# Optimization experiments

Measured on AMD Instinct MI355X. Metric: run time of the kernel, lower is better.

The kernel has to match this reference:

```python
import jax, jax.numpy as jnp
import numpy as np

B, T, D = 4, 1024, 256
H, DK, C = 8, 32, 16  # n_heads, d_key, pos-encoder hidden units
DV = D // H
NEG = -1e15
EPS_SM = 1e-5
EPS_LN = 1e-5
SLOPE = 0.01  # LeakyReLU default


def setup_inputs() -> dict:
    key = jax.random.key(0)
    ks = jax.random.split(key, 16)
    s = 0.05
    x = jax.random.normal(ks[0], (B, T, D), jnp.float32)
    src_mask = jax.random.randint(ks[1], (B, T, T), 0, 2).astype(bool)
    rel_dists = jax.random.uniform(ks[2], (B, 1, T, T), jnp.float32)
    Wq = jax.random.normal(ks[3], (H, DK, D), jnp.float32) * s
    Wk = jax.random.normal(ks[4], (H, DK, D), jnp.float32) * s
    Wv = jax.random.normal(ks[5], (H, DV, D), jnp.float32) * s
    pw1 = jax.random.normal(ks[6], (H, C), jnp.float32) * s
    pb1 = jax.random.normal(ks[7], (H, C), jnp.float32) * s
    pw2 = jax.random.normal(ks[8], (H, C), jnp.float32) * s
    pb2 = jax.random.normal(ks[9], (H,), jnp.float32) * s
    Wo = jax.random.normal(ks[10], (D, D), jnp.float32) * s
    bo = jax.random.normal(ks[11], (D,), jnp.float32) * s
    Wf = jax.random.normal(ks[12], (D, D), jnp.float32) * s
    bf = jax.random.normal(ks[13], (D,), jnp.float32) * s
    g1 = jnp.ones((D,), jnp.float32)
    beta1 = jnp.zeros((D,), jnp.float32)
    g2 = jnp.ones((D,), jnp.float32)
    beta2 = jnp.zeros((D,), jnp.float32)
    return dict(x=x, src_mask=src_mask, rel_dists=rel_dists, Wq=Wq, Wk=Wk, Wv=Wv,
                pw1=pw1, pb1=pb1, pw2=pw2, pb2=pb2, Wo=Wo, bo=bo, Wf=Wf, bf=bf,
                g1=g1, beta1=beta1, g2=g2, beta2=beta2)


def _l2norm(v):
    # F.normalize(p=2, dim=-1): v / max(||v||, 1e-12)
    n = jnp.sqrt(jnp.sum(v * v, axis=-1, keepdims=True))
    return v / jnp.maximum(n, 1e-12)


def _lrelu(h):
    return jnp.where(h >= 0, h, SLOPE * h)


def _pos_bias(d, pw1, pb1, pw2, pb2):
    # d: [B,T,T]; per-head 1x1-conv MLP applied elementwise.
    # Loop over the tiny channel dim (16) to avoid a [B,H,T,T,C] intermediate.
    bias = jnp.broadcast_to(pb2[None, :, None, None], (d.shape[0], pw1.shape[0], d.shape[1], d.shape[2]))
    for c in range(pw1.shape[1]):
        h = d[:, None] * pw1[None, :, c, None, None] + pb1[None, :, c, None, None]
        bias = bias + pw2[None, :, c, None, None] * _lrelu(h)
    return bias  # [B,H,T,T]


def _layer_norm(v, g, b):
    mu = jnp.mean(v, axis=-1, keepdims=True)
    var = jnp.mean((v - mu) ** 2, axis=-1, keepdims=True)
    return (v - mu) * jax.lax.rsqrt(var + EPS_LN) * g + b


def reference(x, src_mask, rel_dists, Wq, Wk, Wv, pw1, pb1, pw2, pb2,
              Wo, bo, Wf, bf, g1, beta1, g2, beta2):
    # cosine-normalized multi-head attention (all heads batched)
    q = _l2norm(jnp.einsum('btd,hkd->bhtk', x, Wq))
    k = _l2norm(jnp.einsum('bsd,hkd->bhsk', x, Wk))
    v = jnp.einsum('bsd,hvd->bhsv', x, Wv)
    logits = jnp.einsum('bhtk,bhsk->bhts', q, k)
    logits = logits - _pos_bias(rel_dists[:, 0], pw1, pb1, pw2, pb2)
    logits = jnp.where(src_mask[:, None], NEG, logits)
    # custom softmax: exp / (sum + 1e-5) (handles all-padded rows)
    z = jnp.exp(logits)
    attn = z / (jnp.sum(z, axis=-1, keepdims=True) + EPS_SM)
    heads = jnp.einsum('bhts,bhsv->bhtv', attn, v)
    y = heads.transpose(0, 2, 1, 3).reshape(x.shape[0], x.shape[1], -1)  # concat heads
    y = y @ Wo.T + bo
    # residual + LN + FFN (dropout is identity in eval mode)
    zz = _layer_norm(x + y, g1, beta1)
    z_ff = _lrelu(zz @ Wf.T + bf)
    return _layer_norm(zz + z_ff, g2, beta2)
```

## Files before the change

### kernel.cpp

```cpp
#include <hip/hip_runtime.h>
#include <math.h>

#define Tc 1024
#define Dc 256
#define Hc 8
#define Cc 16
#define LUTN 256

typedef __attribute__((ext_vector_type(8))) short short8;
typedef __attribute__((ext_vector_type(4))) float f32x4;

__device__ __forceinline__ unsigned bf16u(float x) {
    unsigned u = __float_as_uint(x);
    return (u + 0x7FFFu + ((u >> 16) & 1u)) >> 16;
}
__device__ __forceinline__ unsigned pk2(float lo, float hi) {
    return bf16u(lo) | (bf16u(hi) << 16);
}
__device__ __forceinline__ unsigned pk2t(float lo, float hi) {
    return __builtin_amdgcn_perm(__float_as_uint(hi), __float_as_uint(lo), 0x07060302u);
}
__device__ __forceinline__ float upk(unsigned v) { return __uint_as_float(v << 16); }
__device__ __forceinline__ float upkh(unsigned v) { return __uint_as_float(v & 0xffff0000u); }

__global__ __launch_bounds__(256) void cast_all(
    const float* __restrict__ rel, const int* __restrict__ msk,
    const float* __restrict__ Wq, const float* __restrict__ Wk,
    const float* __restrict__ Wv, const float* __restrict__ Wo,
    const float* __restrict__ Wf,
    const float* __restrict__ pw1, const float* __restrict__ pb1,
    const float* __restrict__ pw2, const float* __restrict__ pb2,
    ushort* __restrict__ Wqkvc, ushort* __restrict__ Woc,
    ushort* __restrict__ Wfc, ushort* __restrict__ LUTb,
    ushort* __restrict__ Dm)
{
    const int bid = blockIdx.x;
    const int tid = threadIdx.x;
    if (bid == 320) {
        const int bin = tid;
        const float d0 = bin * (1.f / LUTN), d1 = (bin + 1) * (1.f / LUTN);
        for (int h = 0; h < Hc; ++h) {
            float y0 = pb2[h], y1 = pb2[h];
#pragma unroll
            for (int c = 0; c < Cc; ++c) {
                float w1 = pw1[h * Cc + c], b1 = pb1[h * Cc + c], w2 = pw2[h * Cc + c];
                float h0 = fmaf(w1, d0, b1), h1 = fmaf(w1, d1, b1);
                y0 = fmaf(w2, h0 >= 0.f ? h0 : 0.01f * h0, y0);
                y1 = fmaf(w2, h1 >= 0.f ? h1 : 0.01f * h1, y1);
            }
            float a = (y1 - y0) * (float)LUTN;
            float b = y0 - a * d0;
            LUTb[(h >> 1) * 1024 + bin * 4 + (h & 1) * 2]     = (ushort)bf16u(a);
            LUTb[(h >> 1) * 1024 + bin * 4 + (h & 1) * 2 + 1] = (ushort)bf16u(b);
        }
        return;
    }
    if (bid < 320) {
        const int e = bid * 1024 + tid * 4;
        const float* src; ushort* dst; int off;
        if      (e <  65536) { src = Wq; dst = Wqkvc;          off = e; }
        else if (e < 131072) { src = Wk; dst = Wqkvc + 65536;  off = e - 65536; }
        else if (e < 196608) { src = Wv; dst = Wqkvc + 131072; off = e - 131072; }
        else if (e < 262144) { src = Wo; dst = Woc;            off = e - 196608; }
        else                 { src = Wf; dst = Wfc;            off = e - 262144; }
        float4 v = *(const float4*)(src + off);
        uint2 p; p.x = pk2(v.x, v.y); p.y = pk2(v.z, v.w);
        *(uint2*)(dst + off) = p;
        return;
    }
    const int idx = (bid - 321) * 1024 + tid * 4;
    float4 d4 = *(const float4*)(rel + idx);
    int4   m4 = *(const int4*)(msk + idx);
    uint2 p;
    p.x = (m4.x ? 0xBF80u : bf16u(d4.x)) | ((m4.y ? 0xBF80u : bf16u(d4.y)) << 16);
    p.y = (m4.z ? 0xBF80u : bf16u(d4.z)) | ((m4.w ? 0xBF80u : bf16u(d4.w)) << 16);
    *(uint2*)(Dm + idx) = p;
}

__global__ __launch_bounds__(256) void qkv_direct(
    const float* __restrict__ x, const ushort* __restrict__ Wqkv,
    ushort* __restrict__ Qb, ushort* __restrict__ Kb, ushort* __restrict__ Vt)
{
    const int tid = threadIdx.x;
    const int w = tid >> 6;
    const int l = tid & 63;
    const int u = l & 15, g = l >> 4;
    const int rbase = blockIdx.x * 16;
    const int cb = (blockIdx.y * 4 + w) * 64;

    f32x4 acc[4];
#pragma unroll
    for (int nt = 0; nt < 4; ++nt) acc[nt] = (f32x4){0.f, 0.f, 0.f, 0.f};

    const float* arow = x + (size_t)(rbase + u) * 256 + g * 8;
#pragma unroll 2
    for (int k0 = 0; k0 < 256; k0 += 32) {
        float4 a0 = *(const float4*)(arow + k0);
        float4 a1 = *(const float4*)(arow + k0 + 4);
        union { short8 s; unsigned wds[4]; } A;
        A.wds[0] = pk2(a0.x, a0.y); A.wds[1] = pk2(a0.z, a0.w);
        A.wds[2] = pk2(a1.x, a1.y); A.wds[3] = pk2(a1.z, a1.w);
#pragma unroll
        for (int nt = 0; nt < 4; ++nt) {
            short8 bfr = *(const short8*)(Wqkv + (size_t)(cb + nt * 16 + u) * 256 + k0 + g * 8);
            acc[nt] = __builtin_amdgcn_mfma_f32_16x16x32_bf16(A.s, bfr, acc[nt], 0, 0, 0);
        }
    }

    const int mat = cb >> 8;
    const int fcb = cb & 255;
    if (mat < 2) {
        ushort* Out = (mat == 0) ? Qb : Kb;
#pragma unroll
        for (int hp = 0; hp < 2; ++hp) {
            const int head = (fcb >> 5) + hp;
#pragma unroll
            for (int reg = 0; reg < 4; ++reg) {
                float ss = acc[2 * hp][reg] * acc[2 * hp][reg]
                         + acc[2 * hp + 1][reg] * acc[2 * hp + 1][reg];
                ss += __shfl_xor(ss, 1, 64);
                ss += __shfl_xor(ss, 2, 64);
                ss += __shfl_xor(ss, 4, 64);
                ss += __shfl_xor(ss, 8, 64);
                float scn = 1.f / fmaxf(sqrtf(ss), 1e-12f);
                const int t = rbase + 4 * g + reg;
                const int bb = t >> 10, tt = t & 1023;
                const size_t base = ((size_t)(bb * 8 + head) * Tc + tt) * 32;
                Out[base + u]      = (ushort)bf16u(acc[2 * hp][reg] * scn);
                Out[base + 16 + u] = (ushort)bf16u(acc[2 * hp + 1][reg] * scn);
            }
        }
    } else {
#pragma unroll
        for (int nt = 0; nt < 4; ++nt) {
            const int head = (fcb >> 5) + (nt >> 1);
            const int vt = nt & 1;
#pragma unroll
            for (int reg = 0; reg < 4; ++reg) {
                const int s = rbase + 4 * g + reg;
                const int bb = s >> 10, ss = s & 1023;
                const int bh = bb * 8 + head;
                Vt[(((size_t)bh * 32 + (ss >> 5)) * 2 + vt) * 512 + u * 32 + (ss & 31)] =
                    (ushort)bf16u(acc[nt][reg]);
            }
        }
    }
}

__global__ __launch_bounds__(256) void attn_mfma(
    const ushort* __restrict__ Qb, const ushort* __restrict__ Kb,
    const ushort* __restrict__ Vt, const ushort* __restrict__ Dm,
    const ushort* __restrict__ LUTb,
    ushort* __restrict__ Yb)
{
    const int tid = threadIdx.x;
    const int w = tid >> 6;
    const int l = tid & 63;
    const int u = l & 15;
    const int g = l >> 4;
    const int t0 = blockIdx.x * 16;
    const int b = blockIdx.y;
    const int hg = blockIdx.z;

    __shared__ __align__(16) ushort lut_s[1024];
    __shared__ __align__(16) unsigned plds[4 * 320];
    __shared__ __align__(16) ushort comb[4 * 16 * 72];
    __shared__ float rs_s[8 * 16];

    if (tid < 128)
        *(uint4*)(lut_s + tid * 8) = *(const uint4*)(LUTb + hg * 1024 + tid * 8);

    const int bh0 = b * 8 + hg * 2;
    short8 qf[2];
#pragma unroll
    for (int hi = 0; hi < 2; ++hi)
        qf[hi] = *(const short8*)(Qb + (((size_t)(bh0 + hi) * Tc + t0 + u) * 32 + g * 8));

    const short8 ones = (short8){0x3F80, 0x3F80, 0x3F80, 0x3F80,
                                 0x3F80, 0x3F80, 0x3F80, 0x3F80};

    f32x4 oacc[2][2];
    f32x4 rsacc[2];
#pragma unroll
    for (int hi = 0; hi < 2; ++hi) {
        oacc[hi][0] = (f32x4){0.f, 0.f, 0.f, 0.f};
        oacc[hi][1] = (f32x4){0.f, 0.f, 0.f, 0.f};
        rsacc[hi]   = (f32x4){0.f, 0.f, 0.f, 0.f};
    }

    unsigned* pwb = plds + w * 320;
    const size_t dbase = (size_t)b * Tc * Tc;

    __syncthreads();

    const int s_begin = w * 256;
    unsigned dmv[4];
#pragma unroll
    for (int reg = 0; reg < 4; ++reg) {
        const int t = t0 + 4 * g + reg;
        dmv[reg] = *(const unsigned*)(Dm + dbase + (size_t)t * Tc + s_begin + 2 * u);
    }

    for (int sc = s_begin; sc < s_begin + 256; sc += 32) {
        unsigned dmn[4] = {0, 0, 0, 0};
        const int nx = sc + 32;
        if (nx < s_begin + 256) {
#pragma unroll
            for (int reg = 0; reg < 4; ++reg) {
                const int t = t0 + 4 * g + reg;
                dmn[reg] = *(const unsigned*)(Dm + dbase + (size_t)t * Tc + nx + 2 * u);
            }
        }
        float dA[4], dB[4];
#pragma unroll
        for (int reg = 0; reg < 4; ++reg) {
            dA[reg] = upk(dmv[reg]);
            dB[reg] = upkh(dmv[reg]);
        }
        float biasA[4][2], biasB[4][2];
#pragma unroll
        for (int reg = 0; reg < 4; ++reg) {
            int iA = (int)(dA[reg] * (float)LUTN);
            int iB = (int)(dB[reg] * (float)LUTN);
            iA = iA < 0 ? 0 : (iA > LUTN - 1 ? LUTN - 1 : iA);
            iB = iB < 0 ? 0 : (iB > LUTN - 1 ? LUTN - 1 : iB);
            uint2 wA = *(const uint2*)(lut_s + iA * 4);
            uint2 wB = *(const uint2*)(lut_s + iB * 4);
            biasA[reg][0] = fmaf(upk(wA.x), dA[reg], upkh(wA.x));
            biasA[reg][1] = fmaf(upk(wA.y), dA[reg], upkh(wA.y));
            biasB[reg][0] = fmaf(upk(wB.x), dB[reg], upkh(wB.x));
            biasB[reg][1] = fmaf(upk(wB.y), dB[reg], upkh(wB.y));
        }
#pragma unroll
        for (int hi = 0; hi < 2; ++hi) {
            const size_t kb = ((size_t)(bh0 + hi) * Tc + sc + 2 * u) * 32 + g * 8;
            short8 kfA = *(const short8*)(Kb + kb);
            short8 kfB = *(const short8*)(Kb + kb + 32);
            const f32x4 z4 = (f32x4){0.f, 0.f, 0.f, 0.f};
            f32x4 sA = __builtin_amdgcn_mfma_f32_16x16x32_bf16(qf[hi], kfA, z4, 0, 0, 0);
            f32x4 sB = __builtin_amdgcn_mfma_f32_16x16x32_bf16(qf[hi], kfB, z4, 0, 0, 0);
#pragma unroll
            for (int reg = 0; reg < 4; ++reg) {
                float zA = (dA[reg] < 0.f) ? 0.f : __expf(sA[reg] - biasA[reg][hi]);
                float zB = (dB[reg] < 0.f) ? 0.f : __expf(sB[reg] - biasB[reg][hi]);
                pwb[(4 * g + reg) * 20 + u] = pk2t(zA, zB);
            }
            short8 pf = *(const short8*)((const char*)pwb + u * 80 + g * 16);
            const ushort* vb = Vt + ((size_t)(bh0 + hi) * 32 + (sc >> 5)) * 1024;
            short8 vf0 = *(const short8*)(vb + u * 32 + g * 8);
            short8 vf1 = *(const short8*)(vb + 512 + u * 32 + g * 8);
            oacc[hi][0] = __builtin_amdgcn_mfma_f32_16x16x32_bf16(pf, vf0, oacc[hi][0], 0, 0, 0);
            oacc[hi][1] = __builtin_amdgcn_mfma_f32_16x16x32_bf16(pf, vf1, oacc[hi][1], 0, 0, 0);
            rsacc[hi]   = __builtin_amdgcn_mfma_f32_16x16x32_bf16(pf, ones, rsacc[hi], 0, 0, 0);
        }
#pragma unroll
        for (int reg = 0; reg < 4; ++reg) dmv[reg] = dmn[reg];
    }

#pragma unroll
    for (int hi = 0; hi < 2; ++hi)
        if (u == 0) {
#pragma unroll
            for (int reg = 0; reg < 4; ++reg)
                rs_s[(w * 2 + hi) * 16 + 4 * g + reg] = rsacc[hi][reg];
        }
#pragma unroll
    for (int hi = 0; hi < 2; ++hi)
#pragma unroll
        for (int vt = 0; vt < 2; ++vt)
#pragma unroll
            for (int reg = 0; reg < 4; ++reg)
                comb[w * 1152 + (4 * g + reg) * 72 + hi * 32 + vt * 16 + u] =
                    (ushort)(__float_as_uint(oacc[hi][vt][reg]) >> 16);
    __syncthreads();

    if (tid < 128) {
        const int tl = tid >> 3;
        const int f0 = (tid & 7) * 8;
        const int hl = f0 >> 5;
        float rstot = rs_s[hl * 16 + tl] + rs_s[(2 + hl) * 16 + tl]
                    + rs_s[(4 + hl) * 16 + tl] + rs_s[(6 + hl) * 16 + tl];
        float inv = 1.f / (rstot + 1e-5f);
        float o[8];
#pragma unroll
        for (int k = 0; k < 8; ++k) o[k] = 0.f;
#pragma unroll
        for (int ww = 0; ww < 4; ++ww) {
            uint4 pv = *(const uint4*)&comb[ww * 1152 + tl * 72 + f0];
            o[0] += upk(pv.x); o[1] += upkh(pv.x);
            o[2] += upk(pv.y); o[3] += upkh(pv.y);
            o[4] += upk(pv.z); o[5] += upkh(pv.z);
            o[6] += upk(pv.w); o[7] += upkh(pv.w);
        }
        uint4 pwv;
        pwv.x = pk2(o[0] * inv, o[1] * inv); pwv.y = pk2(o[2] * inv, o[3] * inv);
        pwv.z = pk2(o[4] * inv, o[5] * inv); pwv.w = pk2(o[6] * inv, o[7] * inv);
        *(uint4*)(Yb + ((size_t)b * Tc + t0 + tl) * Dc + hg * 64 + f0) = pwv;
    }
}

__global__ __launch_bounds__(256) void gemm_ln(
    const ushort* __restrict__ A, const ushort* __restrict__ W,
    const float* __restrict__ bias,
    const float* __restrict__ resF, const ushort* __restrict__ resB,
    const float* __restrict__ gam, const float* __restrict__ bet,
    float* __restrict__ outF, ushort* __restrict__ outB, int act)
{
    const int tid = threadIdx.x;
    const int w = tid >> 6;
    const int l = tid & 63;
    const int u = l & 15, g = l >> 4;
    const int rbase = blockIdx.x * 16;

    __shared__ float red1[64], red2[64];

    f32x4 acc[4];
#pragma unroll
    for (int nt = 0; nt < 4; ++nt) acc[nt] = (f32x4){0.f, 0.f, 0.f, 0.f};

    const ushort* arow = A + (size_t)(rbase + u) * 256 + g * 8;
#pragma unroll 2
    for (int k0 = 0; k0 < 256; k0 += 32) {
        short8 af = *(const short8*)(arow + k0);
#pragma unroll
        for (int nt = 0; nt < 4; ++nt) {
            short8 bfr = *(const short8*)(W + (size_t)(w * 64 + nt * 16 + u) * 256 + k0 + g * 8);
            acc[nt] = __builtin_amdgcn_mfma_f32_16x16x32_bf16(af, bfr, acc[nt], 0, 0, 0);
        }
    }

    float bv[4];
#pragma unroll
    for (int nt = 0; nt < 4; ++nt) bv[nt] = bias[w * 64 + nt * 16 + u];

    float sv[4][4];
#pragma unroll
    for (int reg = 0; reg < 4; ++reg) {
        const int row = rbase + 4 * g + reg;
        float s1 = 0.f, s2 = 0.f;
#pragma unroll
        for (int nt = 0; nt < 4; ++nt) {
            const int col = w * 64 + nt * 16 + u;
            float v = acc[nt][reg] + bv[nt];
            if (act) v = v >= 0.f ? v : 0.01f * v;
            float res = resF ? resF[(size_t)row * 256 + col]
                             : upk((unsigned)resB[(size_t)row * 256 + col]);
            float s = v + res;
            sv[reg][nt] = s;
            s1 += s;
            s2 = fmaf(s, s, s2);
        }
        s1 += __shfl_xor(s1, 1, 64); s2 += __shfl_xor(s2, 1, 64);
        s1 += __shfl_xor(s1, 2, 64); s2 += __shfl_xor(s2, 2, 64);
        s1 += __shfl_xor(s1, 4, 64); s2 += __shfl_xor(s2, 4, 64);
        s1 += __shfl_xor(s1, 8, 64); s2 += __shfl_xor(s2, 8, 64);
        if (u == 0) { red1[w * 16 + 4 * g + reg] = s1; red2[w * 16 + 4 * g + reg] = s2; }
    }
    __syncthreads();

    float gv[4], btv[4];
#pragma unroll
    for (int nt = 0; nt < 4; ++nt) {
        gv[nt]  = gam[w * 64 + nt * 16 + u];
        btv[nt] = bet[w * 64 + nt * 16 + u];
    }
#pragma unroll
    for (int reg = 0; reg < 4; ++reg) {
        const int row = rbase + 4 * g + reg;
        const int rl = 4 * g + reg;
        float S1 = red1[rl] + red1[16 + rl] + red1[32 + rl] + red1[48 + rl];
        float S2 = red2[rl] + red2[16 + rl] + red2[32 + rl] + red2[48 + rl];
        float mu = S1 * (1.f / 256.f);
        float var = S2 * (1.f / 256.f) - mu * mu;
        float rsig = rsqrtf(var + 1e-5f);
#pragma unroll
        for (int nt = 0; nt < 4; ++nt) {
            const int col = w * 64 + nt * 16 + u;
            float o = (sv[reg][nt] - mu) * rsig * gv[nt] + btv[nt];
            if (outF) outF[(size_t)row * 256 + col] = o;
            else      outB[(size_t)row * 256 + col] = (ushort)bf16u(o);
        }
    }
}

extern "C" void kernel_launch(void* const* d_in, const int* in_sizes, int n_in,
                              void* d_out, int out_size, void* d_ws, size_t ws_size,
                              hipStream_t stream) {
    const float* x    = (const float*)d_in[0];
    const int*   mask = (const int*)d_in[1];
    const float* rel  = (const float*)d_in[2];
    const float* Wq   = (const float*)d_in[3];
    const float* Wk   = (const float*)d_in[4];
    const float* Wv   = (const float*)d_in[5];
    const float* pw1  = (const float*)d_in[6];
    const float* pb1  = (const float*)d_in[7];
    const float* pw2  = (const float*)d_in[8];
    const float* pb2  = (const float*)d_in[9];
    const float* Wo   = (const float*)d_in[10];
    const float* bo   = (const float*)d_in[11];
    const float* Wf   = (const float*)d_in[12];
    const float* bf   = (const float*)d_in[13];
    const float* g1   = (const float*)d_in[14];
    const float* be1  = (const float*)d_in[15];
    const float* g2   = (const float*)d_in[16];
    const float* be2  = (const float*)d_in[17];
    float* out = (float*)d_out;

    char* wsb = (char*)d_ws;
    ushort* Qb    = (ushort*)(wsb);
    ushort* Kb    = (ushort*)(wsb + (size_t)( 2 << 20));
    ushort* Vt    = (ushort*)(wsb + (size_t)( 4 << 20));
    ushort* Yb    = (ushort*)(wsb + (size_t)( 6 << 20));
    ushort* Wqkvc = (ushort*)(wsb + (size_t)( 8 << 20));
    ushort* Woc   = (ushort*)(wsb + (size_t)( 8 << 20) + (512 << 10));
    ushort* Wfc   = (ushort*)(wsb + (size_t)( 8 << 20) + (768 << 10));
    ushort* LUTb  = (ushort*)(wsb + (size_t)( 9 << 20));
    ushort* ZZb   = (ushort*)(wsb + (size_t)(10 << 20));
    ushort* Dm    = (ushort*)(wsb + (size_t)(12 << 20));

    cast_all<<<4417, 256, 0, stream>>>(rel, mask, Wq, Wk, Wv, Wo, Wf,
                                       pw1, pb1, pw2, pb2,
                                       Wqkvc, Woc, Wfc, LUTb, Dm);
    qkv_direct<<<dim3(256, 3), 256, 0, stream>>>(x, Wqkvc, Qb, Kb, Vt);
    attn_mfma<<<dim3(64, 4, 4), 256, 0, stream>>>(Qb, Kb, Vt, Dm, LUTb, Yb);
    gemm_ln<<<256, 256, 0, stream>>>(Yb, Woc, bo, x, nullptr, g1, be1,
                                     nullptr, ZZb, 0);
    gemm_ln<<<256, 256, 0, stream>>>(ZZb, Wfc, bf, nullptr, ZZb, g2, be2,
                                     out, nullptr, 1);
}
```

Before: 176.3 us.

## Keep attention probabilities in registers, prefetch K, fuse output GEMM+LN+FFN+LN

```diff
diff --git a/kernel.cpp b/kernel.cpp
--- a/kernel.cpp
+++ b/kernel.cpp
@@ -163,7 +163,6 @@
     const int hg = blockIdx.z;
 
     __shared__ __align__(16) ushort lut_s[1024];
-    __shared__ __align__(16) unsigned plds[4 * 320];
     __shared__ __align__(16) ushort comb[4 * 16 * 72];
     __shared__ float rs_s[8 * 16];
 
@@ -188,73 +187,77 @@
         rsacc[hi]   = (f32x4){0.f, 0.f, 0.f, 0.f};
     }
 
-    unsigned* pwb = plds + w * 320;
-    const size_t dbase = (size_t)b * Tc * Tc;
-
     __syncthreads();
 
     const int s_begin = w * 256;
-    unsigned dmv[4];
-#pragma unroll
-    for (int reg = 0; reg < 4; ++reg) {
-        const int t = t0 + 4 * g + reg;
-        dmv[reg] = *(const unsigned*)(Dm + dbase + (size_t)t * Tc + s_begin + 2 * u);
+    const ushort* drow = Dm + (size_t)b * Tc * Tc + (size_t)(t0 + u) * Tc;
+
+    uint4 dmv = *(const uint4*)(drow + s_begin + 8 * g);
+    short8 kc[2][2];
+#pragma unroll
+    for (int hi = 0; hi < 2; ++hi) {
+        const size_t kb = ((size_t)(bh0 + hi) * Tc + s_begin + 2 * u) * 32 + g * 8;
+        kc[hi][0] = *(const short8*)(Kb + kb);
+        kc[hi][1] = *(const short8*)(Kb + kb + 32);
     }
 
     for (int sc = s_begin; sc < s_begin + 256; sc += 32) {
-        unsigned dmn[4] = {0, 0, 0, 0};
-        const int nx = sc + 32;
-        if (nx < s_begin + 256) {
-#pragma unroll
-            for (int reg = 0; reg < 4; ++reg) {
-                const int t = t0 + 4 * g + reg;
-                dmn[reg] = *(const unsigned*)(Dm + dbase + (size_t)t * Tc + nx + 2 * u);
-            }
-        }
+        const int nx = (sc + 32 < s_begin + 256) ? sc + 32 : s_begin;
+        uint4 dmn = *(const uint4*)(drow + nx + 8 * g);
+        short8 kn[2][2];
+#pragma unroll
+        for (int hi = 0; hi < 2; ++hi) {
+            const size_t kb = ((size_t)(bh0 + hi) * Tc + nx + 2 * u) * 32 + g * 8;
+            kn[hi][0] = *(const short8*)(Kb + kb);
+            kn[hi][1] = *(const short8*)(Kb + kb + 32);
+        }
+
+        const unsigned dw[4] = {dmv.x, dmv.y, dmv.z, dmv.w};
         float dA[4], dB[4];
 #pragma unroll
-        for (int reg = 0; reg < 4; ++reg) {
-            dA[reg] = upk(dmv[reg]);
-            dB[reg] = upkh(dmv[reg]);
+        for (int j = 0; j < 4; ++j) {
+            dA[j] = upk(dw[j]);
+            dB[j] = upkh(dw[j]);
         }
         float biasA[4][2], biasB[4][2];
 #pragma unroll
-        for (int reg = 0; reg < 4; ++reg) {
-            int iA = (int)(dA[reg] * (float)LUTN);
-            int iB = (int)(dB[reg] * (float)LUTN);
+        for (int j = 0; j < 4; ++j) {
+            int iA = (int)(dA[j] * (float)LUTN);
+            int iB = (int)(dB[j] * (float)LUTN);
             iA = iA < 0 ? 0 : (iA > LUTN - 1 ? LUTN - 1 : iA);
             iB = iB < 0 ? 0 : (iB > LUTN - 1 ? LUTN - 1 : iB);
             uint2 wA = *(const uint2*)(lut_s + iA * 4);
             uint2 wB = *(const uint2*)(lut_s + iB * 4);
-            biasA[reg][0] = fmaf(upk(wA.x), dA[reg], upkh(wA.x));
-            biasA[reg][1] = fmaf(upk(wA.y), dA[reg], upkh(wA.y));
-            biasB[reg][0] = fmaf(upk(wB.x), dB[reg], upkh(wB.x));
-            biasB[reg][1] = fmaf(upk(wB.y), dB[reg], upkh(wB.y));
+            biasA[j][0] = fmaf(upk(wA.x), dA[j], upkh(wA.x));
+            biasA[j][1] = fmaf(upk(wA.y), dA[j], upkh(wA.y));
+            biasB[j][0] = fmaf(upk(wB.x), dB[j], upkh(wB.x));
+            biasB[j][1] = fmaf(upk(wB.y), dB[j], upkh(wB.y));
         }
 #pragma unroll
         for (int hi = 0; hi < 2; ++hi) {
-            const size_t kb = ((size_t)(bh0 + hi) * Tc + sc + 2 * u) * 32 + g * 8;
-            short8 kfA = *(const short8*)(Kb + kb);
-            short8 kfB = *(const short8*)(Kb + kb + 32);
             const f32x4 z4 = (f32x4){0.f, 0.f, 0.f, 0.f};
-            f32x4 sA = __builtin_amdgcn_mfma_f32_16x16x32_bf16(qf[hi], kfA, z4, 0, 0, 0);
-            f32x4 sB = __builtin_amdgcn_mfma_f32_16x16x32_bf16(qf[hi], kfB, z4, 0, 0, 0);
-#pragma unroll
-            for (int reg = 0; reg < 4; ++reg) {
-                float zA = (dA[reg] < 0.f) ? 0.f : __expf(sA[reg] - biasA[reg][hi]);
-                float zB = (dB[reg] < 0.f) ? 0.f : __expf(sB[reg] - biasB[reg][hi]);
-                pwb[(4 * g + reg) * 20 + u] = pk2t(zA, zB);
+            f32x4 sA = __builtin_amdgcn_mfma_f32_16x16x32_bf16(kc[hi][0], qf[hi], z4, 0, 0, 0);
+            f32x4 sB = __builtin_amdgcn_mfma_f32_16x16x32_bf16(kc[hi][1], qf[hi], z4, 0, 0, 0);
+            union { short8 s; unsigned w4[4]; } P;
+#pragma unroll
+            for (int j = 0; j < 4; ++j) {
+                float zA = (dA[j] < 0.f) ? 0.f : __expf(sA[j] - biasA[j][hi]);
+                float zB = (dB[j] < 0.f) ? 0.f : __expf(sB[j] - biasB[j][hi]);
+                P.w4[j] = pk2t(zA, zB);
             }
-            short8 pf = *(const short8*)((const char*)pwb + u * 80 + g * 16);
             const ushort* vb = Vt + ((size_t)(bh0 + hi) * 32 + (sc >> 5)) * 1024;
             short8 vf0 = *(const short8*)(vb + u * 32 + g * 8);
             short8 vf1 = *(const short8*)(vb + 512 + u * 32 + g * 8);
-            oacc[hi][0] = __builtin_amdgcn_mfma_f32_16x16x32_bf16(pf, vf0, oacc[hi][0], 0, 0, 0);
-            oacc[hi][1] = __builtin_amdgcn_mfma_f32_16x16x32_bf16(pf, vf1, oacc[hi][1], 0, 0, 0);
-            rsacc[hi]   = __builtin_amdgcn_mfma_f32_16x16x32_bf16(pf, ones, rsacc[hi], 0, 0, 0);
-        }
-#pragma unroll
-        for (int reg = 0; reg < 4; ++reg) dmv[reg] = dmn[reg];
+            oacc[hi][0] = __builtin_amdgcn_mfma_f32_16x16x32_bf16(P.s, vf0, oacc[hi][0], 0, 0, 0);
+            oacc[hi][1] = __builtin_amdgcn_mfma_f32_16x16x32_bf16(P.s, vf1, oacc[hi][1], 0, 0, 0);
+            rsacc[hi]   = __builtin_amdgcn_mfma_f32_16x16x32_bf16(P.s, ones, rsacc[hi], 0, 0, 0);
+        }
+        dmv = dmn;
+#pragma unroll
+        for (int hi = 0; hi < 2; ++hi) {
+            kc[hi][0] = kn[hi][0];
+            kc[hi][1] = kn[hi][1];
+        }
     }
 
 #pragma unroll
@@ -299,12 +302,13 @@
     }
 }
 
-__global__ __launch_bounds__(256) void gemm_ln(
-    const ushort* __restrict__ A, const ushort* __restrict__ W,
-    const float* __restrict__ bias,
-    const float* __restrict__ resF, const ushort* __restrict__ resB,
-    const float* __restrict__ gam, const float* __restrict__ bet,
-    float* __restrict__ outF, ushort* __restrict__ outB, int act)
+__global__ __launch_bounds__(512) void out_fused(
+    const ushort* __restrict__ Yb, const ushort* __restrict__ Woc,
+    const float* __restrict__ bo, const float* __restrict__ x,
+    const float* __restrict__ g1, const float* __restrict__ be1,
+    const ushort* __restrict__ Wfc, const float* __restrict__ bfb,
+    const float* __restrict__ g2, const float* __restrict__ be2,
+    float* __restrict__ out)
 {
     const int tid = threadIdx.x;
     const int w = tid >> 6;
@@ -312,40 +316,36 @@
     const int u = l & 15, g = l >> 4;
     const int rbase = blockIdx.x * 16;
 
-    __shared__ float red1[64], red2[64];
-
-    f32x4 acc[4];
-#pragma unroll
-    for (int nt = 0; nt < 4; ++nt) acc[nt] = (f32x4){0.f, 0.f, 0.f, 0.f};
-
-    const ushort* arow = A + (size_t)(rbase + u) * 256 + g * 8;
+    __shared__ float red1[128], red2[128];
+    __shared__ __align__(16) ushort ZZs[16 * 256];
+
+    f32x4 acc[2];
+    acc[0] = (f32x4){0.f, 0.f, 0.f, 0.f};
+    acc[1] = (f32x4){0.f, 0.f, 0.f, 0.f};
+    const ushort* arow = Yb + (size_t)(rbase + u) * 256 + g * 8;
 #pragma unroll 2
     for (int k0 = 0; k0 < 256; k0 += 32) {
         short8 af = *(const short8*)(arow + k0);
 #pragma unroll
-        for (int nt = 0; nt < 4; ++nt) {
-            short8 bfr = *(const short8*)(W + (size_t)(w * 64 + nt * 16 + u) * 256 + k0 + g * 8);
+        for (int nt = 0; nt < 2; ++nt) {
+            short8 bfr = *(const short8*)(Woc + (size_t)(w * 32 + nt * 16 + u) * 256 + k0 + g * 8);
             acc[nt] = __builtin_amdgcn_mfma_f32_16x16x32_bf16(af, bfr, acc[nt], 0, 0, 0);
         }
     }
 
-    float bv[4];
-#pragma unroll
-    for (int nt = 0; nt < 4; ++nt) bv[nt] = bias[w * 64 + nt * 16 + u];
-
-    float sv[4][4];
+    float bv[2];
+#pragma unroll
+    for (int nt = 0; nt < 2; ++nt) bv[nt] = bo[w * 32 + nt * 16 + u];
+
+    float sv[4][2];
 #pragma unroll
     for (int reg = 0; reg < 4; ++reg) {
         const int row = rbase + 4 * g + reg;
         float s1 = 0.f, s2 = 0.f;
 #pragma unroll
-        for (int nt = 0; nt < 4; ++nt) {
-            const int col = w * 64 + nt * 16 + u;
-            float v = acc[nt][reg] + bv[nt];
-            if (act) v = v >= 0.f ? v : 0.01f * v;
-            float res = resF ? resF[(size_t)row * 256 + col]
-                             : upk((unsigned)resB[(size_t)row * 256 + col]);
-            float s = v + res;
+        for (int nt = 0; nt < 2; ++nt) {
+            const int col = w * 32 + nt * 16 + u;
+            float s = acc[nt][reg] + bv[nt] + x[(size_t)row * 256 + col];
             sv[reg][nt] = s;
             s1 += s;
             s2 = fmaf(s, s, s2);
@@ -358,27 +358,80 @@
     }
     __syncthreads();
 
-    float gv[4], btv[4];
-#pragma unroll
-    for (int nt = 0; nt < 4; ++nt) {
-        gv[nt]  = gam[w * 64 + nt * 16 + u];
-        btv[nt] = bet[w * 64 + nt * 16 + u];
-    }
+    float zzv[4][2];
+#pragma unroll
+    for (int reg = 0; reg < 4; ++reg) {
+        const int rl = 4 * g + reg;
+        float S1 = 0.f, S2 = 0.f;
+#pragma unroll
+        for (int ww = 0; ww < 8; ++ww) { S1 += red1[ww * 16 + rl]; S2 += red2[ww * 16 + rl]; }
+        float mu = S1 * (1.f / 256.f);
+        float var = S2 * (1.f / 256.f) - mu * mu;
+        float rsig = rsqrtf(var + 1e-5f);
+#pragma unroll
+        for (int nt = 0; nt < 2; ++nt) {
+            const int col = w * 32 + nt * 16 + u;
+            float zz = (sv[reg][nt] - mu) * rsig * g1[col] + be1[col];
+            zzv[reg][nt] = zz;
+            const int boff = (rl * 512 + col * 2) ^ ((rl & 7) << 4);
+            *(ushort*)((char*)ZZs + boff) = (ushort)bf16u(zz);
+        }
+    }
+    __syncthreads();
+
+    f32x4 acc2[2];
+    acc2[0] = (f32x4){0.f, 0.f, 0.f, 0.f};
+    acc2[1] = (f32x4){0.f, 0.f, 0.f, 0.f};
+#pragma unroll 2
+    for (int k0 = 0; k0 < 256; k0 += 32) {
+        const int aoff = (u * 512 + (k0 + g * 8) * 2) ^ ((u & 7) << 4);
+        short8 af = *(const short8*)((const char*)ZZs + aoff);
+#pragma unroll
+        for (int nt = 0; nt < 2; ++nt) {
+            short8 bfr = *(const short8*)(Wfc + (size_t)(w * 32 + nt * 16 + u) * 256 + k0 + g * 8);
+            acc2[nt] = __builtin_amdgcn_mfma_f32_16x16x32_bf16(af, bfr, acc2[nt], 0, 0, 0);
+        }
+    }
+
+    float bv2[2];
+#pragma unroll
+    for (int nt = 0; nt < 2; ++nt) bv2[nt] = bfb[w * 32 + nt * 16 + u];
+
+    float sv2[4][2];
+#pragma unroll
+    for (int reg = 0; reg < 4; ++reg) {
+        float s1 = 0.f, s2 = 0.f;
+#pragma unroll
+        for (int nt = 0; nt < 2; ++nt) {
+            float v = acc2[nt][reg] + bv2[nt];
+            v = v >= 0.f ? v : 0.01f * v;
+            float s = v + zzv[reg][nt];
+            sv2[reg][nt] = s;
+            s1 += s;
+            s2 = fmaf(s, s, s2);
+        }
+        s1 += __shfl_xor(s1, 1, 64); s2 += __shfl_xor(s2, 1, 64);
+        s1 += __shfl_xor(s1, 2, 64); s2 += __shfl_xor(s2, 2, 64);
+        s1 += __shfl_xor(s1, 4, 64); s2 += __shfl_xor(s2, 4, 64);
+        s1 += __shfl_xor(s1, 8, 64); s2 += __shfl_xor(s2, 8, 64);
+        if (u == 0) { red1[w * 16 + 4 * g + reg] = s1; red2[w * 16 + 4 * g + reg] = s2; }
+    }
+    __syncthreads();
+
 #pragma unroll
     for (int reg = 0; reg < 4; ++reg) {
         const int row = rbase + 4 * g + reg;
         const int rl = 4 * g + reg;
-        float S1 = red1[rl] + red1[16 + rl] + red1[32 + rl] + red1[48 + rl];
-        float S2 = red2[rl] + red2[16 + rl] + red2[32 + rl] + red2[48 + rl];
+        float S1 = 0.f, S2 = 0.f;
+#pragma unroll
+        for (int ww = 0; ww < 8; ++ww) { S1 += red1[ww * 16 + rl]; S2 += red2[ww * 16 + rl]; }
         float mu = S1 * (1.f / 256.f);
         float var = S2 * (1.f / 256.f) - mu * mu;
         float rsig = rsqrtf(var + 1e-5f);
 #pragma unroll
-        for (int nt = 0; nt < 4; ++nt) {
-            const int col = w * 64 + nt * 16 + u;
-            float o = (sv[reg][nt] - mu) * rsig * gv[nt] + btv[nt];
-            if (outF) outF[(size_t)row * 256 + col] = o;
-            else      outB[(size_t)row * 256 + col] = (ushort)bf16u(o);
+        for (int nt = 0; nt < 2; ++nt) {
+            const int col = w * 32 + nt * 16 + u;
+            out[(size_t)row * 256 + col] = (sv2[reg][nt] - mu) * rsig * g2[col] + be2[col];
         }
     }
 }
@@ -415,16 +468,13 @@
     ushort* Woc   = (ushort*)(wsb + (size_t)( 8 << 20) + (512 << 10));
     ushort* Wfc   = (ushort*)(wsb + (size_t)( 8 << 20) + (768 << 10));
     ushort* LUTb  = (ushort*)(wsb + (size_t)( 9 << 20));
-    ushort* ZZb   = (ushort*)(wsb + (size_t)(10 << 20));
-    ushort* Dm    = (ushort*)(wsb + (size_t)(12 << 20));
+    ushort* Dm    = (ushort*)(wsb + (size_t)(10 << 20));
 
     cast_all<<<4417, 256, 0, stream>>>(rel, mask, Wq, Wk, Wv, Wo, Wf,
                                        pw1, pb1, pw2, pb2,
                                        Wqkvc, Woc, Wfc, LUTb, Dm);
     qkv_direct<<<dim3(256, 3), 256, 0, stream>>>(x, Wqkvc, Qb, Kb, Vt);
     attn_mfma<<<dim3(64, 4, 4), 256, 0, stream>>>(Qb, Kb, Vt, Dm, LUTb, Yb);
-    gemm_ln<<<256, 256, 0, stream>>>(Yb, Woc, bo, x, nullptr, g1, be1,
-                                     nullptr, ZZb, 0);
-    gemm_ln<<<256, 256, 0, stream>>>(ZZb, Wfc, bf, nullptr, ZZb, g2, be2,
-                                     out, nullptr, 1);
-}
+    out_fused<<<256, 512, 0, stream>>>(Yb, Woc, bo, x, g1, be1,
+                                       Wfc, bf, g2, be2, out);
+}
```

Result: no change. 178.8 us (+1.4%).
